# Performance work log

Hardware: AMD Instinct MI355X
Metric: run time of the kernel (lower is better)

The kernel has to match this reference:

```python
import jax, jax.numpy as jnp
import numpy as np

B, W, N = 4, 8, 1024
F_IN, HID, OUT = 256, 256, 128


def setup_inputs() -> dict:
    key = jax.random.key(0)
    ks = jax.random.split(key, 8)
    X = jax.random.normal(ks[0], (B, W, N, F_IN), dtype=jnp.float32)
    adj = jax.random.uniform(ks[1], (B, W, N, N), dtype=jnp.float32)
    # Linear params, torch default init: U(-1/sqrt(fan_in), 1/sqrt(fan_in))
    def lin(k, fi, fo):
        k1, k2 = jax.random.split(k)
        bnd = 1.0 / np.sqrt(fi)
        Wm = jax.random.uniform(k1, (fi, fo), minval=-bnd, maxval=bnd, dtype=jnp.float32)
        bm = jax.random.uniform(k2, (fo,), minval=-bnd, maxval=bnd, dtype=jnp.float32)
        return Wm, bm
    W1, b1 = lin(ks[2], F_IN, HID)
    W2, b2 = lin(ks[3], HID, HID)
    W3, b3 = lin(ks[4], HID, OUT)
    return {"X": X, "adj": adj, "W1": W1, "b1": b1, "W2": W2, "b2": b2, "W3": W3, "b3": b3}


def _normalize(adj):
    # adj: [B, W, N, N]. adj_hat = adj + I; sym degree norm D^-1/2 A D^-1/2
    n = adj.shape[-1]
    adj_hat = adj + jnp.eye(n, dtype=adj.dtype)
    d = jnp.sum(adj_hat, axis=-1) ** (-0.5)            # [B, W, N]
    # diag(d) @ adj_hat @ diag(d) == row/col scaling (same math, no N^3 diag matmuls)
    return adj_hat * d[..., :, None] * d[..., None, :]


def reference(X, adj, W1, b1, W2, b2, W3, b3):
    adj_norm = _normalize(adj)                          # [B, W, N, N]
    h = X
    for Wm, bm in ((W1, b1), (W2, b2), (W3, b3)):
        h = jnp.einsum('bwnm,bwmf->bwnf', adj_norm, h)  # aggregate
        h = jax.nn.relu(jnp.einsum('bwnf,fo->bwno', h, Wm) + bm)
    return h                                            # [B, W, N, OUT]
```

## Files before the change

kernel.cpp:

```cpp
#include <hip/hip_runtime.h>
#include <hip/hip_bf16.h>
#include <cstdint>
#include <cstddef>

#define NN 1024
#define FF 256

typedef __attribute__((ext_vector_type(8))) short bf16x8;
typedef __attribute__((ext_vector_type(4))) float f32x4;

__device__ __forceinline__ short f2bf(float x) {
  unsigned int u = __float_as_uint(x);
  u = (u + 0x7fffu + ((u >> 16) & 1u)) >> 16;
  return (short)u;
}


__global__ __launch_bounds__(256)
void dinv_cast(const float* __restrict__ adj, float* __restrict__ dinv,
               short* __restrict__ Ahat) {
  __shared__ float wsum[64];
  int b = blockIdx.x;
  int bw = b >> 6, s = b & 63;
  int t = threadIdx.x;
  int wid = t >> 6, lane = t & 63;
  int row = lane & 15;
  int rloc = (s << 4) + row;
  int kg = (lane >> 4) & 3;
  const float* arow = adj + ((size_t)(bw << 10) + rloc) * NN;
  short* outb = Ahat + ((size_t)bw << 20) + ((size_t)s << 14) + (t << 3);
  float ssum = 0.f;
  #pragma unroll
  for (int it = 0; it < 8; it++) {
    int col = (it << 7) + (wid << 5) + (kg << 3);
    float4 a0 = *(const float4*)(arow + col);
    float4 a1 = *(const float4*)(arow + col + 4);
    float v[8] = {a0.x, a0.y, a0.z, a0.w, a1.x, a1.y, a1.z, a1.w};
    union { ushort o[8]; int4 q; } pk;
    #pragma unroll
    for (int j = 0; j < 8; j++) {
      v[j] += (rloc == col + j) ? 1.f : 0.f;
      ssum += v[j];
      pk.o[j] = (ushort)f2bf(v[j]);
    }
    *(int4*)(outb + (it << 11)) = pk.q;
  }
  ssum += __shfl_down(ssum, 32, 64);
  ssum += __shfl_down(ssum, 16, 64);
  if (lane < 16) wsum[(wid << 4) + lane] = ssum;
  __syncthreads();
  if (t < 16) {
    float tot = wsum[t] + wsum[16 + t] + wsum[32 + t] + wsum[48 + t];
    dinv[(bw << 10) + (s << 4) + t] = rsqrtf(tot);
  }
}

__global__ __launch_bounds__(256)
void transpose_x(const float* __restrict__ X, const float* __restrict__ dinv,
                 short* __restrict__ XT) {
  __shared__ short T[64][72];
  int bwo = blockIdx.z;
  int n0 = blockIdx.x << 6, f0 = blockIdx.y << 6;
  int t = threadIdx.x;
  {
    int n = t >> 2, fc = (t & 3) << 4;
    float dn = dinv[(bwo << 10) + n0 + n];
    const float* src = X + (((size_t)bwo * NN + n0 + n) * FF) + f0 + fc;
    #pragma unroll
    for (int i = 0; i < 4; i++) {
      float4 v = ((const float4*)src)[i];
      ushort4 p;
      p.x = (unsigned short)f2bf(v.x * dn); p.y = (unsigned short)f2bf(v.y * dn);
      p.z = (unsigned short)f2bf(v.z * dn); p.w = (unsigned short)f2bf(v.w * dn);
      *(ushort4*)&T[n][fc + (i << 2)] = p;
    }
  }
  __syncthreads();
  {
    int f = t >> 2, nc = (t & 3) << 4;
    int fg = f0 + f, ng = n0 + nc;
    short tmp[16];
    #pragma unroll
    for (int i = 0; i < 16; i++) tmp[i] = T[nc + i][f];
    size_t e0 = ((size_t)bwo << 18) + ((size_t)(fg >> 4) << 14) + ((ng >> 5) << 9)
              + (((ng & 31) >> 3) << 7) + ((fg & 15) << 3);
    *(int4*)(XT + e0)       = *(int4*)&tmp[0];
    *(int4*)(XT + e0 + 128) = *(int4*)&tmp[8];
  }
}

__global__ __launch_bounds__(256)
void transpose_w(const float* __restrict__ W, short* __restrict__ WT, int FO) {
  int idx = blockIdx.x * 256 + threadIdx.x;
  if (idx >= FO * 256) return;
  int fo = idx >> 8, fi = idx & 255;
  size_t e = (size_t)((fo >> 4) << 12) + ((fi >> 5) << 9)
           + (((fi & 31) >> 3) << 7) + ((fo & 15) << 3) + (fi & 7);
  WT[e] = f2bf(W[fi * FO + fo]);
}

template<int F_OUT, bool FINAL>
__global__ __launch_bounds__(512, 2)
void gcn_layer(const short* __restrict__ Ahat,
               const float* __restrict__ dinv,
               const short* __restrict__ Gin,
               const short* __restrict__ WT,
               const float* __restrict__ bias,
               short* __restrict__ Gout,
               float* __restrict__ Out) {
  __shared__ short aggL[128 * 272];

  int b = blockIdx.x;
  int x = b & 7, m = b >> 3;
  int bw = (x << 2) + (m >> 3);
  int rb = m & 7;
  int r0 = rb << 7;

  int tid = threadIdx.x;
  int wid = tid >> 6, lane = tid & 63;
  int l15 = lane & 15, l4 = lane >> 4;
  int wr = wid >> 2, wf = wid & 3;

  const short* Hb = Gin  + ((size_t)bw << 18) + ((size_t)(wf << 2) << 14) + (lane << 3);
  const short* Ab = Ahat + ((size_t)bw << 20)
                  + ((size_t)((rb << 3) + (wr << 2)) << 14) + (lane << 3);
  const float* dvB = dinv + (bw << 10);

  f32x4 acc[4][4];
  #pragma unroll
  for (int ah = 0; ah < 4; ah++)
    #pragma unroll
    for (int aa = 0; aa < 4; aa++) acc[ah][aa] = f32x4{0.f, 0.f, 0.f, 0.f};

  bf16x8 hE[4], aE[4], hO[4], aO[4];

#define LD(HB, AB, T)                                                         \
  {                                                                           \
    _Pragma("unroll")                                                         \
    for (int ah = 0; ah < 4; ah++)                                            \
      HB[ah] = *(const bf16x8*)(Hb + ah * 16384 + (T) * 512);                 \
    _Pragma("unroll")                                                         \
    for (int aa = 0; aa < 4; aa++)                                            \
      AB[aa] = *(const bf16x8*)(Ab + aa * 16384 + (T) * 512);                 \
  }
#define MM(HB, AB)                                                            \
  __builtin_amdgcn_s_setprio(1);                                              \
  _Pragma("unroll")                                                           \
  for (int ah = 0; ah < 4; ah++)                                              \
    _Pragma("unroll")                                                         \
    for (int aa = 0; aa < 4; aa++)                                            \
      acc[ah][aa] = __builtin_amdgcn_mfma_f32_16x16x32_bf16(                  \
          HB[ah], AB[aa], acc[ah][aa], 0, 0, 0);                              \
  __builtin_amdgcn_s_setprio(0);

  LD(hE, aE, 0);
  LD(hO, aO, 1);
  #pragma unroll
  for (int it = 0; it < 16; ++it) {
    __builtin_amdgcn_s_barrier();
    MM(hE, aE);
    if (it < 15) LD(hE, aE, 2 * it + 2);
    MM(hO, aO);
    if (it < 15) LD(hO, aO, 2 * it + 3);
  }
#undef LD
#undef MM

  float dsc[4];
  #pragma unroll
  for (int aa = 0; aa < 4; aa++) dsc[aa] = dvB[r0 + (wr << 6) + (aa << 4) + l15];
  #pragma unroll
  for (int ah = 0; ah < 4; ah++)
    #pragma unroll
    for (int aa = 0; aa < 4; aa++) {
      int r = (wr << 6) + (aa << 4) + l15;
      int fB = ((wf << 6) + (ah << 4) + (l4 << 2)) << 1;
      int off = (r * 544 + (fB ^ ((r & 7) << 4))) >> 1;
      ushort4 p;
      p.x = (unsigned short)f2bf(acc[ah][aa][0] * dsc[aa]);
      p.y = (unsigned short)f2bf(acc[ah][aa][1] * dsc[aa]);
      p.z = (unsigned short)f2bf(acc[ah][aa][2] * dsc[aa]);
      p.w = (unsigned short)f2bf(acc[ah][aa][3] * dsc[aa]);
      *(ushort4*)(aggL + off) = p;
    }
  __syncthreads();

  constexpr int NFO = F_OUT / 64;
  const short* Wbase = WT + (size_t)(wf * NFO) * 4096 + (lane << 3);
  f32x4 acc2[4][NFO];
  #pragma unroll
  for (int am = 0; am < 4; am++)
    #pragma unroll
    for (int nf = 0; nf < NFO; nf++) acc2[am][nf] = f32x4{0.f, 0.f, 0.f, 0.f};

  #pragma unroll
  for (int kt = 0; kt < 8; kt++) {
    bf16x8 af[4];
    #pragma unroll
    for (int am = 0; am < 4; am++) {
      int r = (wr << 6) + (am << 4) + l15;
      int fB = (kt << 6) + (l4 << 4);
      af[am] = *(const bf16x8*)(aggL + ((r * 544 + (fB ^ ((r & 7) << 4))) >> 1));
    }
    #pragma unroll
    for (int nf = 0; nf < NFO; nf++) {
      bf16x8 wv = *(const bf16x8*)(Wbase + (size_t)nf * 4096 + (kt << 9));
      #pragma unroll
      for (int am = 0; am < 4; am++)
        acc2[am][nf] = __builtin_amdgcn_mfma_f32_16x16x32_bf16(af[am], wv, acc2[am][nf], 0, 0, 0);
    }
  }

  #pragma unroll
  for (int am = 0; am < 4; am++) {
    int nodeLoc = (wr << 6) + (am << 4) + (l4 << 2);
    float4 dn4 = *(const float4*)(dvB + r0 + nodeLoc);
    float dn[4] = {dn4.x, dn4.y, dn4.z, dn4.w};
    #pragma unroll
    for (int nf = 0; nf < NFO; nf++) {
      int fo = wf * (F_OUT / 4) + (nf << 4) + l15;
      float bb = bias[fo];
      float v[4];
      #pragma unroll
      for (int j = 0; j < 4; j++) v[j] = fmaxf(acc2[am][nf][j] + bb, 0.f);
      if (!FINAL) {
        ushort4 p;
        p.x = (unsigned short)f2bf(v[0] * dn[0]);
        p.y = (unsigned short)f2bf(v[1] * dn[1]);
        p.z = (unsigned short)f2bf(v[2] * dn[2]);
        p.w = (unsigned short)f2bf(v[3] * dn[3]);
        size_t e = (size_t)bw * (F_OUT * 1024) + ((size_t)(fo >> 4) << 14)
                 + ((size_t)((rb << 2) + (wr << 1) + (am >> 1)) << 9)
                 + ((size_t)(((am & 1) << 1) + (l4 >> 1)) << 7)
                 + ((fo & 15) << 3) + ((l4 & 1) << 2);
        *(ushort4*)(Gout + e) = p;
      } else {
        float* ob = Out + ((size_t)(bw << 10) + r0 + nodeLoc) * F_OUT + fo;
        ob[0]         = v[0];
        ob[F_OUT]     = v[1];
        ob[2 * F_OUT] = v[2];
        ob[3 * F_OUT] = v[3];
      }
    }
  }
}

extern "C" void kernel_launch(void* const* d_in, const int* in_sizes, int n_in,
                              void* d_out, int out_size, void* d_ws, size_t ws_size,
                              hipStream_t stream) {
  const float* X   = (const float*)d_in[0];
  const float* adj = (const float*)d_in[1];
  const float* W1  = (const float*)d_in[2];
  const float* b1  = (const float*)d_in[3];
  const float* W2  = (const float*)d_in[4];
  const float* b2  = (const float*)d_in[5];
  const float* W3  = (const float*)d_in[6];
  const float* b3  = (const float*)d_in[7];
  float* out = (float*)d_out;

  char* ws = (char*)d_ws;
  float* dinv = (float*)ws;
  short* WT1  = (short*)(ws + 131072);
  short* WT2  = (short*)(ws + 262144);
  short* WT3  = (short*)(ws + 393216);
  short* bufA = (short*)(ws + 458752);
  short* bufB = (short*)(ws + 458752 + 16777216);
  short* Ahat = (short*)(ws + 458752 + 2 * 16777216);

  dinv_cast<<<2048, 256, 0, stream>>>(adj, dinv, Ahat);
  transpose_x<<<dim3(16, 4, 32), 256, 0, stream>>>(X, dinv, bufA);
  transpose_w<<<256, 256, 0, stream>>>(W1, WT1, 256);
  transpose_w<<<256, 256, 0, stream>>>(W2, WT2, 256);
  transpose_w<<<128, 256, 0, stream>>>(W3, WT3, 128);

  gcn_layer<256, false><<<256, 512, 0, stream>>>(Ahat, dinv, bufA, WT1, b1, bufB, nullptr);
  gcn_layer<256, false><<<256, 512, 0, stream>>>(Ahat, dinv, bufB, WT2, b2, bufA, nullptr);
  gcn_layer<128, true ><<<256, 512, 0, stream>>>(Ahat, dinv, bufA, WT3, b3, nullptr, out);
}
```

Measured before the change: 140.1 us.

## Triple-buffer aggregation loads without barriers and merge weight transposes into one launch

The aggregation main loop moves from two register buffers to three, so each tile is loaded two MFMA groups ahead of its use. The per-iteration s_barrier that kept waves in step is removed. Separately, the three weight-transpose launches become a single kernel that picks the matrix from the thread index, saving two launches. The extra buffers raise VGPR pressure under the 512x2 launch bounds, and dropping the barrier may hurt cache sharing between waves.

```diff
diff --git a/kernel.cpp b/kernel.cpp
--- a/kernel.cpp
+++ b/kernel.cpp
@@ -90,13 +90,21 @@
 }
 
 __global__ __launch_bounds__(256)
-void transpose_w(const float* __restrict__ W, short* __restrict__ WT, int FO) {
+void transpose_w3(const float* __restrict__ W1, const float* __restrict__ W2,
+                  const float* __restrict__ W3,
+                  short* __restrict__ T1, short* __restrict__ T2,
+                  short* __restrict__ T3) {
   int idx = blockIdx.x * 256 + threadIdx.x;
-  if (idx >= FO * 256) return;
-  int fo = idx >> 8, fi = idx & 255;
+  const float* W; short* T; int FO; int loc;
+  if (idx < 65536)       { W = W1; T = T1; FO = 256; loc = idx; }
+  else if (idx < 131072) { W = W2; T = T2; FO = 256; loc = idx - 65536; }
+  else                   { W = W3; T = T3; FO = 128; loc = idx - 131072; }
+  int fo = (FO == 256) ? (loc >> 8) : (loc >> 8);
+  fo = loc >> 8; int fi = loc & 255;
+  if (fo >= FO) return;
   size_t e = (size_t)((fo >> 4) << 12) + ((fi >> 5) << 9)
            + (((fi & 31) >> 3) << 7) + ((fo & 15) << 3) + (fi & 7);
-  WT[e] = f2bf(W[fi * FO + fo]);
+  T[e] = f2bf(W[fi * FO + fo]);
 }
 
 template<int F_OUT, bool FINAL>
@@ -132,7 +140,7 @@
     #pragma unroll
     for (int aa = 0; aa < 4; aa++) acc[ah][aa] = f32x4{0.f, 0.f, 0.f, 0.f};
 
-  bf16x8 hE[4], aE[4], hO[4], aO[4];
+  bf16x8 h0[4], a0[4], h1[4], a1[4], h2[4], a2[4];
 
 #define LD(HB, AB, T)                                                         \
   {                                                                           \
@@ -153,16 +161,20 @@
           HB[ah], AB[aa], acc[ah][aa], 0, 0, 0);                              \
   __builtin_amdgcn_s_setprio(0);
 
-  LD(hE, aE, 0);
-  LD(hO, aO, 1);
-  #pragma unroll
-  for (int it = 0; it < 16; ++it) {
-    __builtin_amdgcn_s_barrier();
-    MM(hE, aE);
-    if (it < 15) LD(hE, aE, 2 * it + 2);
-    MM(hO, aO);
-    if (it < 15) LD(hO, aO, 2 * it + 3);
-  }
+  LD(h0, a0, 0);
+  LD(h1, a1, 1);
+  LD(h2, a2, 2);
+  #pragma unroll
+  for (int it = 0; it < 10; ++it) {
+    MM(h0, a0);
+    if (3 * it + 3 < 32) LD(h0, a0, 3 * it + 3);
+    MM(h1, a1);
+    if (3 * it + 4 < 32) LD(h1, a1, 3 * it + 4);
+    MM(h2, a2);
+    if (3 * it + 5 < 32) LD(h2, a2, 3 * it + 5);
+  }
+  MM(h0, a0);
+  MM(h1, a1);
 #undef LD
 #undef MM
 
@@ -268,10 +280,8 @@
   short* Ahat = (short*)(ws + 458752 + 2 * 16777216);
 
   dinv_cast<<<2048, 256, 0, stream>>>(adj, dinv, Ahat);
+  transpose_w3<<<640, 256, 0, stream>>>(W1, W2, W3, WT1, WT2, WT3);
   transpose_x<<<dim3(16, 4, 32), 256, 0, stream>>>(X, dinv, bufA);
-  transpose_w<<<256, 256, 0, stream>>>(W1, WT1, 256);
-  transpose_w<<<256, 256, 0, stream>>>(W2, WT2, 256);
-  transpose_w<<<128, 256, 0, stream>>>(W3, WT3, 128);
 
   gcn_layer<256, false><<<256, 512, 0, stream>>>(Ahat, dinv, bufA, WT1, b1, bufB, nullptr);
   gcn_layer<256, false><<<256, 512, 0, stream>>>(Ahat, dinv, bufB, WT2, b2, bufA, nullptr);
```

Measured after the change: 135.3 us. -3.4%, faster.

## Stage adjacency tiles through LDS via async global_load_lds and merge preprocessing launches

Applied to the files above, without the earlier changes.

The aggregation loop now double-buffers the adjacency tile in shared memory using direct global-to-LDS loads, so the four waves in a row group read one shared copy instead of each fetching A from global memory. H operands still come from global into registers, and explicit vmcnt waits plus barriers order the pipeline. The X transpose and the three weight transposes are merged into one kernel to cut launch overhead. The launch-bounds occupancy hint of 2 is dropped, which may change register allocation, and the hand-tuned waitcnt counts are fragile.

```diff
diff --git a/kernel.cpp b/kernel.cpp
--- a/kernel.cpp
+++ b/kernel.cpp
@@ -8,6 +8,9 @@
 
 typedef __attribute__((ext_vector_type(8))) short bf16x8;
 typedef __attribute__((ext_vector_type(4))) float f32x4;
+
+typedef __attribute__((address_space(1))) const void* gas_ptr;
+typedef __attribute__((address_space(3))) void* las_ptr;
 
 __device__ __forceinline__ short f2bf(float x) {
   unsigned int u = __float_as_uint(x);
@@ -56,51 +59,60 @@
 }
 
 __global__ __launch_bounds__(256)
-void transpose_x(const float* __restrict__ X, const float* __restrict__ dinv,
-                 short* __restrict__ XT) {
+void preproc_xw(const float* __restrict__ X, const float* __restrict__ dinv,
+                short* __restrict__ XT,
+                const float* __restrict__ W1, const float* __restrict__ W2,
+                const float* __restrict__ W3,
+                short* __restrict__ T1, short* __restrict__ T2,
+                short* __restrict__ T3) {
   __shared__ short T[64][72];
-  int bwo = blockIdx.z;
-  int n0 = blockIdx.x << 6, f0 = blockIdx.y << 6;
+  int b = blockIdx.x;
   int t = threadIdx.x;
-  {
-    int n = t >> 2, fc = (t & 3) << 4;
-    float dn = dinv[(bwo << 10) + n0 + n];
-    const float* src = X + (((size_t)bwo * NN + n0 + n) * FF) + f0 + fc;
-    #pragma unroll
-    for (int i = 0; i < 4; i++) {
-      float4 v = ((const float4*)src)[i];
-      ushort4 p;
-      p.x = (unsigned short)f2bf(v.x * dn); p.y = (unsigned short)f2bf(v.y * dn);
-      p.z = (unsigned short)f2bf(v.z * dn); p.w = (unsigned short)f2bf(v.w * dn);
-      *(ushort4*)&T[n][fc + (i << 2)] = p;
-    }
-  }
-  __syncthreads();
-  {
-    int f = t >> 2, nc = (t & 3) << 4;
-    int fg = f0 + f, ng = n0 + nc;
-    short tmp[16];
-    #pragma unroll
-    for (int i = 0; i < 16; i++) tmp[i] = T[nc + i][f];
-    size_t e0 = ((size_t)bwo << 18) + ((size_t)(fg >> 4) << 14) + ((ng >> 5) << 9)
-              + (((ng & 31) >> 3) << 7) + ((fg & 15) << 3);
-    *(int4*)(XT + e0)       = *(int4*)&tmp[0];
-    *(int4*)(XT + e0 + 128) = *(int4*)&tmp[8];
-  }
-}
-
-__global__ __launch_bounds__(256)
-void transpose_w(const float* __restrict__ W, short* __restrict__ WT, int FO) {
-  int idx = blockIdx.x * 256 + threadIdx.x;
-  if (idx >= FO * 256) return;
-  int fo = idx >> 8, fi = idx & 255;
-  size_t e = (size_t)((fo >> 4) << 12) + ((fi >> 5) << 9)
-           + (((fi & 31) >> 3) << 7) + ((fo & 15) << 3) + (fi & 7);
-  WT[e] = f2bf(W[fi * FO + fo]);
+  if (b < 2048) {
+    int bwo = b >> 6;
+    int n0 = (b & 15) << 6, f0 = ((b >> 4) & 3) << 6;
+    {
+      int n = t >> 2, fc = (t & 3) << 4;
+      float dn = dinv[(bwo << 10) + n0 + n];
+      const float* src = X + (((size_t)bwo * NN + n0 + n) * FF) + f0 + fc;
+      #pragma unroll
+      for (int i = 0; i < 4; i++) {
+        float4 v = ((const float4*)src)[i];
+        ushort4 p;
+        p.x = (unsigned short)f2bf(v.x * dn); p.y = (unsigned short)f2bf(v.y * dn);
+        p.z = (unsigned short)f2bf(v.z * dn); p.w = (unsigned short)f2bf(v.w * dn);
+        *(ushort4*)&T[n][fc + (i << 2)] = p;
+      }
+    }
+    __syncthreads();
+    {
+      int f = t >> 2, nc = (t & 3) << 4;
+      int fg = f0 + f, ng = n0 + nc;
+      short tmp[16];
+      #pragma unroll
+      for (int i = 0; i < 16; i++) tmp[i] = T[nc + i][f];
+      size_t e0 = ((size_t)bwo << 18) + ((size_t)(fg >> 4) << 14) + ((ng >> 5) << 9)
+                + (((ng & 31) >> 3) << 7) + ((fg & 15) << 3);
+      *(int4*)(XT + e0)       = *(int4*)&tmp[0];
+      *(int4*)(XT + e0 + 128) = *(int4*)&tmp[8];
+    }
+  } else {
+    int idx = (b - 2048) * 256 + t;
+    const float* W; short* Td; int FO; int loc;
+    if (idx < 65536)       { W = W1; Td = T1; FO = 256; loc = idx; }
+    else if (idx < 131072) { W = W2; Td = T2; FO = 256; loc = idx - 65536; }
+    else                   { W = W3; Td = T3; FO = 128; loc = idx - 131072; }
+    int fo = loc >> 8, fi = loc & 255;
+    if (fo < FO) {
+      size_t e = (size_t)((fo >> 4) << 12) + ((fi >> 5) << 9)
+               + (((fi & 31) >> 3) << 7) + ((fo & 15) << 3) + (fi & 7);
+      Td[e] = f2bf(W[fi * FO + fo]);
+    }
+  }
 }
 
 template<int F_OUT, bool FINAL>
-__global__ __launch_bounds__(512, 2)
+__global__ __launch_bounds__(512)
 void gcn_layer(const short* __restrict__ Ahat,
                const float* __restrict__ dinv,
                const short* __restrict__ Gin,
@@ -108,7 +120,7 @@
                const float* __restrict__ bias,
                short* __restrict__ Gout,
                float* __restrict__ Out) {
-  __shared__ short aggL[128 * 272];
+  __shared__ __align__(16) short lds[34816];
 
   int b = blockIdx.x;
   int x = b & 7, m = b >> 3;
@@ -121,10 +133,21 @@
   int l15 = lane & 15, l4 = lane >> 4;
   int wr = wid >> 2, wf = wid & 3;
 
-  const short* Hb = Gin  + ((size_t)bw << 18) + ((size_t)(wf << 2) << 14) + (lane << 3);
-  const short* Ab = Ahat + ((size_t)bw << 20)
-                  + ((size_t)((rb << 3) + (wr << 2)) << 14) + (lane << 3);
   const float* dvB = dinv + (bw << 10);
+  const short* Hb = Gin + ((size_t)bw << 18) + ((size_t)(wf << 2) << 14) + (lane << 3);
+  const short* Abase = Ahat + ((size_t)bw << 20) + ((size_t)(rb << 3) << 14);
+
+  auto stageA = [&](int sel, int t) {
+    char* base = (char*)lds + (sel << 14);
+    #pragma unroll
+    for (int i = 0; i < 2; i++) {
+      int slot = (i << 9) + tid;
+      int c = slot >> 6, o = slot & 63;
+      const short* g = Abase + ((size_t)(c >> 1) << 14)
+                     + ((size_t)((t << 1) + (c & 1)) << 9) + (o << 3);
+      __builtin_amdgcn_global_load_lds((gas_ptr)g, (las_ptr)(base + (slot << 4)), 16, 0, 0);
+    }
+  };
 
   f32x4 acc[4][4];
   #pragma unroll
@@ -132,40 +155,75 @@
     #pragma unroll
     for (int aa = 0; aa < 4; aa++) acc[ah][aa] = f32x4{0.f, 0.f, 0.f, 0.f};
 
-  bf16x8 hE[4], aE[4], hO[4], aO[4];
-
-#define LD(HB, AB, T)                                                         \
-  {                                                                           \
+  bf16x8 hE[4][2], hO[4][2];
+
+#define LOADH(HB, T)                                                          \
+  { _Pragma("unroll")                                                         \
+    for (int ah = 0; ah < 4; ah++) {                                          \
+      HB[ah][0] = *(const bf16x8*)(Hb + ah * 16384 + (size_t)(2 * (T)) * 512);\
+      HB[ah][1] = *(const bf16x8*)(Hb + ah * 16384 + (size_t)(2 * (T) + 1) * 512); } }
+
+#define DSREADA(AB, PAR)                                                      \
+  { const char* ab_ = (const char*)lds + ((PAR) << 14);                       \
     _Pragma("unroll")                                                         \
-    for (int ah = 0; ah < 4; ah++)                                            \
-      HB[ah] = *(const bf16x8*)(Hb + ah * 16384 + (T) * 512);                 \
-    _Pragma("unroll")                                                         \
-    for (int aa = 0; aa < 4; aa++)                                            \
-      AB[aa] = *(const bf16x8*)(Ab + aa * 16384 + (T) * 512);                 \
-  }
+    for (int aa = 0; aa < 4; aa++) {                                          \
+      int c_ = ((wr << 2) + aa) << 1;                                         \
+      AB[aa][0] = *(const bf16x8*)(ab_ + (c_ << 10) + (lane << 4));           \
+      AB[aa][1] = *(const bf16x8*)(ab_ + ((c_ + 1) << 10) + (lane << 4)); } }
+
 #define MM(HB, AB)                                                            \
   __builtin_amdgcn_s_setprio(1);                                              \
   _Pragma("unroll")                                                           \
-  for (int ah = 0; ah < 4; ah++)                                              \
+  for (int kt = 0; kt < 2; kt++)                                              \
     _Pragma("unroll")                                                         \
-    for (int aa = 0; aa < 4; aa++)                                            \
-      acc[ah][aa] = __builtin_amdgcn_mfma_f32_16x16x32_bf16(                  \
-          HB[ah], AB[aa], acc[ah][aa], 0, 0, 0);                              \
+    for (int ah = 0; ah < 4; ah++)                                            \
+      _Pragma("unroll")                                                       \
+      for (int aa = 0; aa < 4; aa++)                                          \
+        acc[ah][aa] = __builtin_amdgcn_mfma_f32_16x16x32_bf16(                \
+            HB[ah][kt], AB[aa][kt], acc[ah][aa], 0, 0, 0);                    \
   __builtin_amdgcn_s_setprio(0);
 
-  LD(hE, aE, 0);
-  LD(hO, aO, 1);
-  #pragma unroll
-  for (int it = 0; it < 16; ++it) {
+  stageA(0, 0);
+  __builtin_amdgcn_sched_barrier(0);
+  LOADH(hE, 0);
+  asm volatile("s_waitcnt vmcnt(8)" ::: "memory");
+  __builtin_amdgcn_sched_barrier(0);
+  __builtin_amdgcn_s_barrier();
+
+  #pragma unroll
+  for (int it = 0; it < 8; ++it) {
+    const int t0 = 2 * it, t1 = t0 + 1;
+    if (t0 < 15) stageA(1, t1);
+    __builtin_amdgcn_sched_barrier(0);
+    if (t0 < 15) LOADH(hO, t1);
+    {
+      bf16x8 aF[4][2];
+      DSREADA(aF, 0);
+      MM(hE, aF);
+    }
+    if (t0 < 15) { asm volatile("s_waitcnt vmcnt(8)" ::: "memory"); }
+    else         { asm volatile("s_waitcnt vmcnt(0)" ::: "memory"); }
+    __builtin_amdgcn_sched_barrier(0);
     __builtin_amdgcn_s_barrier();
-    MM(hE, aE);
-    if (it < 15) LD(hE, aE, 2 * it + 2);
-    MM(hO, aO);
-    if (it < 15) LD(hO, aO, 2 * it + 3);
-  }
-#undef LD
+    if (t1 > 15) break;
+    if (t1 < 15) stageA(0, t1 + 1);
+    __builtin_amdgcn_sched_barrier(0);
+    if (t1 < 15) LOADH(hE, t1 + 1);
+    {
+      bf16x8 aG[4][2];
+      DSREADA(aG, 1);
+      MM(hO, aG);
+    }
+    if (t1 < 15) { asm volatile("s_waitcnt vmcnt(8)" ::: "memory"); }
+    else         { asm volatile("s_waitcnt vmcnt(0)" ::: "memory"); }
+    __builtin_amdgcn_sched_barrier(0);
+    __builtin_amdgcn_s_barrier();
+  }
+#undef LOADH
+#undef DSREADA
 #undef MM
 
+  short* aggL = lds;
   float dsc[4];
   #pragma unroll
   for (int aa = 0; aa < 4; aa++) dsc[aa] = dvB[r0 + (wr << 6) + (aa << 4) + l15];
@@ -268,10 +326,7 @@
   short* Ahat = (short*)(ws + 458752 + 2 * 16777216);
 
   dinv_cast<<<2048, 256, 0, stream>>>(adj, dinv, Ahat);
-  transpose_x<<<dim3(16, 4, 32), 256, 0, stream>>>(X, dinv, bufA);
-  transpose_w<<<256, 256, 0, stream>>>(W1, WT1, 256);
-  transpose_w<<<256, 256, 0, stream>>>(W2, WT2, 256);
-  transpose_w<<<128, 256, 0, stream>>>(W3, WT3, 128);
+  preproc_xw<<<2688, 256, 0, stream>>>(X, dinv, bufA, W1, W2, W3, WT1, WT2, WT3);
 
   gcn_layer<256, false><<<256, 512, 0, stream>>>(Ahat, dinv, bufA, WT1, b1, bufB, nullptr);
   gcn_layer<256, false><<<256, 512, 0, stream>>>(Ahat, dinv, bufB, WT2, b2, bufA, nullptr);
```

Result: faster. 135.4 us (-3.4%).
